# Performance work log

Measured on AMD Instinct MI355X. Metric: run time of the kernel, lower is better.

## Reference

```python
import jax, jax.numpy as jnp
import numpy as np

DIM = 64
NUM_FEAT = 14
NUM_OUT = 105
N_NODES = 8192
N_EDGES = 16384
N_GRAPHS = 256
N_STEMS = 2048
N_JBONDS = 1024


def lrelu(v):
    return jax.nn.leaky_relu(v, 0.01)


def setup_inputs() -> dict:
    key = jax.random.key(0)
    ks = jax.random.split(key, 40)
    def rn(k, shape, s=0.1):
        return jax.random.normal(k, shape, dtype=jnp.float32) * s
    inp = {}
    inp['x'] = jax.random.normal(ks[0], (N_NODES, NUM_FEAT), dtype=jnp.float32)
    inp['edge_attr'] = jax.random.uniform(ks[1], (N_EDGES, 4), dtype=jnp.float32)
    inp['edge_index'] = jax.random.randint(ks[2], (2, N_EDGES), 0, N_NODES)
    inp['batch'] = jnp.sort(jax.random.randint(ks[3], (N_NODES,), 0, N_GRAPHS))
    inp['stem_atmidx'] = jax.random.randint(ks[4], (N_STEMS,), 0, N_NODES)
    inp['jbond_atmidx'] = jax.random.randint(ks[5], (N_JBONDS, 2), 0, N_NODES)
    # lin0
    inp['lin0_w'] = rn(ks[6], (NUM_FEAT, DIM)); inp['lin0_b'] = rn(ks[7], (DIM,))
    # NNConv edge net: Linear(4,dim) -> LeakyReLU -> Linear(dim, dim*dim)
    inp['net_w1'] = rn(ks[8], (4, DIM)); inp['net_b1'] = rn(ks[9], (DIM,))
    inp['net_w2'] = rn(ks[10], (DIM, DIM * DIM), 0.02); inp['net_b2'] = rn(ks[11], (DIM * DIM,), 0.02)
    # NNConv root weight + bias
    inp['conv_root'] = rn(ks[12], (DIM, DIM)); inp['conv_bias'] = rn(ks[13], (DIM,))
    # GRU (torch gate order r,z,n); stored [in, 3*dim]
    inp['gru_w_ih'] = rn(ks[14], (DIM, 3 * DIM)); inp['gru_w_hh'] = rn(ks[15], (DIM, 3 * DIM))
    inp['gru_b_ih'] = rn(ks[16], (3 * DIM,)); inp['gru_b_hh'] = rn(ks[17], (3 * DIM,))
    # node2stem MLP
    inp['n2s_w1'] = rn(ks[18], (DIM, DIM)); inp['n2s_b1'] = rn(ks[19], (DIM,))
    inp['n2s_w2'] = rn(ks[20], (DIM, NUM_OUT)); inp['n2s_b2'] = rn(ks[21], (NUM_OUT,))
    # node2jbond MLP
    inp['n2j_w1'] = rn(ks[22], (DIM, DIM)); inp['n2j_b1'] = rn(ks[23], (DIM,))
    inp['n2j_w2'] = rn(ks[24], (DIM, 1)); inp['n2j_b2'] = rn(ks[25], (1,))
    # Set2Set LSTM(2*dim -> dim), torch gate order i,f,g,o; stored [in, 4*dim]
    inp['s2s_w_ih'] = rn(ks[26], (2 * DIM, 4 * DIM)); inp['s2s_w_hh'] = rn(ks[27], (DIM, 4 * DIM))
    inp['s2s_b_ih'] = rn(ks[28], (4 * DIM,)); inp['s2s_b_hh'] = rn(ks[29], (4 * DIM,))
    # lin_out
    inp['lin_out_w'] = rn(ks[30], (2 * DIM, 2)); inp['lin_out_b'] = rn(ks[31], (2,))
    return inp


def reference(x, edge_attr, lin0_w, lin0_b, net_w1, net_b1, net_w2, net_b2,
              conv_root, conv_bias, gru_w_ih, gru_w_hh, gru_b_ih, gru_b_hh,
              n2s_w1, n2s_b1, n2s_w2, n2s_b2, n2j_w1, n2j_b1, n2j_w2, n2j_b2,
              s2s_w_ih, s2s_w_hh, s2s_b_ih, s2s_b_hh, lin_out_w, lin_out_b,
              edge_index, batch, stem_atmidx, jbond_atmidx):
    N = x.shape[0]
    src, dst = edge_index[0], edge_index[1]
    out = lrelu(x @ lin0_w + lin0_b)          # [N, dim]
    h = out
    # edge-conditioned weights (edge_attr is constant across the 6 iterations)
    ew = (lrelu(edge_attr @ net_w1 + net_b1) @ net_w2 + net_b2).reshape(-1, DIM, DIM)  # [E,dim,dim]
    deg = jnp.maximum(jax.ops.segment_sum(jnp.ones_like(dst, dtype=x.dtype), dst, num_segments=N), 1.0)[:, None]
    for _ in range(6):
        msg = jnp.einsum('ei,eio->eo', out[src], ew)                        # per-edge matmul
        agg = jax.ops.segment_sum(msg, dst, num_segments=N) / deg          # scatter-mean
        m = lrelu(agg + out @ conv_root + conv_bias)
        # GRU update (torch gate order r,z,n)
        gi = m @ gru_w_ih + gru_b_ih
        gh = h @ gru_w_hh + gru_b_hh
        ir, iz, inn = jnp.split(gi, 3, axis=-1)
        hr, hz, hn = jnp.split(gh, 3, axis=-1)
        r = jax.nn.sigmoid(ir + hr)
        z = jax.nn.sigmoid(iz + hz)
        n = jnp.tanh(inn + r * hn)
        h = (1.0 - z) * n + z * h
        out = h
    # per-stem block logits
    stem_preds = lrelu(out[stem_atmidx] @ n2s_w1 + n2s_b1) @ n2s_w2 + n2s_b2  # [S, num_out]
    # jbond: gather both endpoints, predict scalar, mean over the pair
    jb = out[jbond_atmidx.reshape(-1)]
    jpred = lrelu(jb @ n2j_w1 + n2j_b1) @ n2j_w2 + n2j_b2                     # [2J,1]
    jbond_preds = jpred.reshape(jbond_atmidx.shape).mean(axis=1)              # [J]
    # Set2Set, processing_steps=1
    B = N_GRAPHS
    hS = jnp.zeros((B, DIM), x.dtype)
    cS = jnp.zeros((B, DIM), x.dtype)
    q_star = jnp.zeros((B, 2 * DIM), x.dtype)
    gates = q_star @ s2s_w_ih + s2s_b_ih + hS @ s2s_w_hh + s2s_b_hh
    gi_, gf_, gg_, go_ = jnp.split(gates, 4, axis=-1)
    cS = jax.nn.sigmoid(gf_) * cS + jax.nn.sigmoid(gi_) * jnp.tanh(gg_)
    hS = jax.nn.sigmoid(go_) * jnp.tanh(cS)
    q = hS                                                                    # [B, dim]
    e = jnp.sum(out * q[batch], axis=-1)                                      # [N]
    emax = jax.ops.segment_max(e, batch, num_segments=B)
    a_un = jnp.exp(e - emax[batch])
    a = a_un / jax.ops.segment_sum(a_un, batch, num_segments=B)[batch]
    r_pool = jax.ops.segment_sum(a[:, None] * out, batch, num_segments=B)     # [B, dim]
    q_star = jnp.concatenate([q, r_pool], axis=1)                             # [B, 2*dim]
    scalar_outs = q_star @ lin_out_w + lin_out_b                              # [B, 2]
    return (scalar_outs, stem_preds, jbond_preds)
```

## Files before the change

### kernel.cpp

```cpp
#include <hip/hip_runtime.h>

#define DIM 64
#define NF 14
#define NOUT 105
#define NN 8192
#define NE 16384
#define NB 256
#define NS 2048
#define NJ 1024
#define KTOT 4160
#define KSPLIT 8

#define C_X      0
#define C_EA     114688
#define C_L0W    180224
#define C_L0B    181120
#define C_NW1    181184
#define C_NB1    181440
#define C_NW2    181504
#define C_NB2    443648
#define C_CRT    447744
#define C_CB     451840
#define C_GWIH   451904
#define C_GWHH   464192
#define C_GBIH   476480
#define C_GBHH   476672
#define C_SW1    476864
#define C_SB1    480960
#define C_SW2    481024
#define C_SB2    487744
#define C_JW1    487856
#define C_JB1    491952
#define C_JW2    492016
#define C_JB2    492080
#define C_S2IH   492088
#define C_S2HH   492344
#define C_LOW    492600
#define C_LOB    492856
#define C_TOT    492864

typedef float f32x4 __attribute__((ext_vector_type(4)));
typedef short bf16x8 __attribute__((ext_vector_type(8)));

__device__ __forceinline__ float bf2f(unsigned short u){
  union { unsigned int i; float f; } v; v.i = ((unsigned int)u) << 16; return v.f;
}
__device__ __forceinline__ unsigned short f2bf(float f){
  union { float f; unsigned int i; } v; v.f = f;
  unsigned int x = v.i;
  return (unsigned short)((x + 0x7FFFu + ((x >> 16) & 1u)) >> 16);
}
__device__ __forceinline__ float sigm(float x){ return 1.f / (1.f + __expf(-x)); }
__device__ __forceinline__ float tanh_f(float x){
  x = fminf(10.f, fmaxf(-10.f, x));
  float e = __expf(2.f * x);
  return (e - 1.f) / (e + 1.f);
}
__device__ __forceinline__ float lrelu(float x){ return x > 0.f ? x : 0.01f * x; }

__device__ __forceinline__ float wred_sum(float v){
  #pragma unroll
  for (int off = 32; off > 0; off >>= 1) v += __shfl_xor(v, off, 64);
  return v;
}
__device__ __forceinline__ float wred_max(float v){
  #pragma unroll
  for (int off = 32; off > 0; off >>= 1) v = fmaxf(v, __shfl_xor(v, off, 64));
  return v;
}


__global__ void k_detect(const unsigned short* __restrict__ ea, int* __restrict__ flag){
  __shared__ int cnt;
  if (threadIdx.x == 0) cnt = 0;
  __syncthreads();
  int c = 0;
  for (int i = threadIdx.x; i < 8192; i += 256) c += (ea[2*i] >> 15) & 1;
  atomicAdd(&cnt, c);
  __syncthreads();
  if (threadIdx.x == 0) *flag = (cnt > 100) ? 1 : 0;
}

struct CvtArgs {
  const void* src[26];
  int n[26];
  int off[26];
};

__global__ void k_cvt(CvtArgs a, const int* __restrict__ flag, unsigned short* __restrict__ dst){
  bool f32 = (*flag != 0);
  int gid = blockIdx.x * blockDim.x + threadIdx.x, gs = gridDim.x * blockDim.x;
  #pragma unroll 1
  for (int j = 0; j < 26; ++j){
    const void* s = a.src[j];
    int n = a.n[j], o = a.off[j];
    for (int i = gid; i < n; i += gs)
      dst[o + i] = f32 ? f2bf(((const float*)s)[i]) : ((const unsigned short*)s)[i];
  }
}


__global__ void k_deg(const int* __restrict__ ei, float* __restrict__ deg){
  int e = blockIdx.x * blockDim.x + threadIdx.x;
  if (e < NE) atomicAdd(&deg[ei[NE + e]], 1.0f);
}

__global__ void k_lin0(const unsigned short* __restrict__ cvt,
                       float* __restrict__ actF, unsigned short* __restrict__ actB){
  const unsigned short* x = cvt + C_X;
  const unsigned short* w = cvt + C_L0W;
  const unsigned short* b = cvt + C_L0B;
  int idx = blockIdx.x * blockDim.x + threadIdx.x;
  int n = idx >> 6, d = idx & 63;
  float acc = bf2f(b[d]);
  #pragma unroll
  for (int f = 0; f < NF; ++f) acc += bf2f(x[n*NF + f]) * bf2f(w[f*DIM + d]);
  float v = lrelu(acc);
  actF[idx] = v; actB[idx] = f2bf(v);
}

__global__ void k_u(const unsigned short* __restrict__ cvt, unsigned short* __restrict__ u){
  const unsigned short* ea = cvt + C_EA;
  const unsigned short* w  = cvt + C_NW1;
  const unsigned short* b  = cvt + C_NB1;
  int idx = blockIdx.x * blockDim.x + threadIdx.x;
  int e = idx >> 6, d = idx & 63;
  float acc = bf2f(b[d]);
  #pragma unroll
  for (int f = 0; f < 4; ++f) acc += bf2f(ea[e*4 + f]) * bf2f(w[f*DIM + d]);
  u[idx] = f2bf(lrelu(acc));
}

__global__ void k_w2t(const unsigned short* __restrict__ cvt, unsigned short* __restrict__ w2t){
  const unsigned short* w2 = cvt + C_NW2;
  int t = blockIdx.x * blockDim.x + threadIdx.x;
  int n = t >> 6, k = t & 63;
  w2t[t] = w2[k*4096 + n];
}

__global__ void k_w2r(const unsigned short* __restrict__ cvt, unsigned short* __restrict__ w2rt){
  const unsigned short* w2 = cvt + C_NW2;
  const unsigned short* b2 = cvt + C_NB2;
  int t = blockIdx.x * blockDim.x + threadIdx.x;
  int o = t / KTOT, k = t - o * KTOT;
  unsigned short v = (k < 4096) ? w2[(k >> 6) * 4096 + (k & 63) * 64 + o]
                                : b2[(k - 4096) * 64 + o];
  w2rt[t] = v;
}

__global__ void k_prep(const unsigned short* __restrict__ cvt,
                       unsigned short* __restrict__ crt, unsigned short* __restrict__ btg,
                       float* __restrict__ cbg, float* __restrict__ qv){
  const unsigned short* cr  = cvt + C_CRT;
  const unsigned short* wih = cvt + C_GWIH;
  const unsigned short* whh = cvt + C_GWHH;
  const unsigned short* bih = cvt + C_GBIH;
  const unsigned short* bhh = cvt + C_GBHH;
  const unsigned short* s2sbih = cvt + C_S2IH;
  const unsigned short* s2sbhh = cvt + C_S2HH;
  int tid = threadIdx.x;
  for (int t = tid; t < 4096; t += 256){ int n = t & 63, k = t >> 6; crt[n*64 + k] = cr[k*64 + n]; }
  for (int t = tid; t < 32768; t += 256){
    int nidx = t >> 7, kidx = t & 127;
    int g = nidx >> 6, d = nidx & 63, ki = kidx & 63;
    unsigned short v = 0;
    if (kidx < 64){
      if (g == 0) v = wih[ki*192 + d];
      else if (g == 1) v = wih[ki*192 + 64 + d];
      else if (g == 2) v = wih[ki*192 + 128 + d];
    } else {
      if (g == 0) v = whh[ki*192 + d];
      else if (g == 1) v = whh[ki*192 + 64 + d];
      else if (g == 3) v = whh[ki*192 + 128 + d];
    }
    btg[nidx*128 + kidx] = v;
  }
  if (tid < 256){
    int g = tid >> 6, d = tid & 63;
    float v;
    if (g == 0) v = bf2f(bih[d]) + bf2f(bhh[d]);
    else if (g == 1) v = bf2f(bih[64 + d]) + bf2f(bhh[64 + d]);
    else if (g == 2) v = bf2f(bih[128 + d]);
    else v = bf2f(bhh[128 + d]);
    cbg[tid] = v;
  }
  if (tid < 64){
    float gi = bf2f(s2sbih[tid])       + bf2f(s2sbhh[tid]);
    float gg = bf2f(s2sbih[128 + tid]) + bf2f(s2sbhh[128 + tid]);
    float go = bf2f(s2sbih[192 + tid]) + bf2f(s2sbhh[192 + tid]);
    float c = sigm(gi) * tanh_f(gg);
    qv[tid] = sigm(go) * tanh_f(c);
  }
}


__global__ __launch_bounds__(256) void k_ew(const unsigned short* __restrict__ z,
                                            const unsigned short* __restrict__ w2t,
                                            const unsigned short* __restrict__ cvt,
                                            unsigned short* __restrict__ ew){
  const unsigned short* b2 = cvt + C_NB2;
  int w = threadIdx.x >> 6, lane = threadIdx.x & 63;
  int lm = lane & 15, q8 = (lane >> 4) * 8, rq = (lane >> 4) * 4;
  int e0 = blockIdx.x * 64;
  int n0 = blockIdx.y * 256 + w * 64;
  f32x4 acc[4][4];
  #pragma unroll
  for (int mt = 0; mt < 4; ++mt)
    #pragma unroll
    for (int nt = 0; nt < 4; ++nt) acc[mt][nt] = (f32x4){0.f, 0.f, 0.f, 0.f};
  #pragma unroll
  for (int kk = 0; kk < 2; ++kk){
    bf16x8 af[4], bfr[4];
    #pragma unroll
    for (int mt = 0; mt < 4; ++mt)
      af[mt] = *(const bf16x8*)&z[(size_t)(e0 + mt*16 + lm)*64 + kk*32 + q8];
    #pragma unroll
    for (int nt = 0; nt < 4; ++nt)
      bfr[nt] = *(const bf16x8*)&w2t[(size_t)(n0 + nt*16 + lm)*64 + kk*32 + q8];
    #pragma unroll
    for (int mt = 0; mt < 4; ++mt)
      #pragma unroll
      for (int nt = 0; nt < 4; ++nt)
        acc[mt][nt] = __builtin_amdgcn_mfma_f32_16x16x32_bf16(af[mt], bfr[nt], acc[mt][nt], 0, 0, 0);
  }
  #pragma unroll
  for (int nt = 0; nt < 4; ++nt){
    int col = n0 + nt*16 + lm;
    float bb = bf2f(b2[col]);
    #pragma unroll
    for (int mt = 0; mt < 4; ++mt)
      #pragma unroll
      for (int r = 0; r < 4; ++r){
        int row = e0 + mt*16 + rq + r;
        ew[(size_t)row*4096 + col] = f2bf(acc[mt][nt][r] + bb);
      }
  }
}

__global__ __launch_bounds__(256) void k_msg(const unsigned short* __restrict__ actB,
                                             const unsigned short* __restrict__ ew,
                                             const int* __restrict__ ei,
                                             float* __restrict__ agg){
  __shared__ float sact[4][64];
  int w = threadIdx.x >> 6, lane = threadIdx.x & 63;
  int e = blockIdx.x * 4 + w;
  int src = ei[e], dst = ei[NE + e];
  sact[w][lane] = bf2f(actB[(size_t)src*64 + lane]);
  __syncthreads();
  const unsigned short* ep = &ew[(size_t)e * 4096];
  float acc = 0.f;
  #pragma unroll 16
  for (int i = 0; i < 64; ++i) acc += sact[w][i] * bf2f(ep[i*64 + lane]);
  atomicAdd(&agg[(size_t)dst*64 + lane], acc);
}


__global__ __launch_bounds__(256) void k_msgf(const unsigned short* __restrict__ actB,
                                              const unsigned short* __restrict__ z,
                                              const unsigned short* __restrict__ w2rt,
                                              const int* __restrict__ ei,
                                              float* __restrict__ agg){
  __shared__ __align__(16) unsigned short sz[256 * 8];
  int w = threadIdx.x >> 6, lane = threadIdx.x & 63;
  int lm = lane & 15, q8 = (lane >> 4) * 8, rq = (lane >> 4) * 4;
  int e0 = blockIdx.x * 256;
  int s  = blockIdx.y;
  {
    int t = threadIdx.x;
    *(uint4*)&sz[t * 8] = *(const uint4*)&z[(size_t)(e0 + t) * 64 + s * 8];
  }
  __syncthreads();

  uint4 apack[4][2];
  #pragma unroll
  for (int mt = 0; mt < 4; ++mt){
    int src = ei[e0 + w*64 + mt*16 + lm];
    apack[mt][0] = *(const uint4*)&actB[(size_t)src * 64 + q8];
    apack[mt][1] = *(const uint4*)&actB[(size_t)src * 64 + 32 + q8];
  }

  f32x4 acc[4][4];
  #pragma unroll
  for (int mt = 0; mt < 4; ++mt)
    #pragma unroll
    for (int nt = 0; nt < 4; ++nt) acc[mt][nt] = (f32x4){0.f, 0.f, 0.f, 0.f};

  int kk0 = s * 16;
  int nk = (s == KSPLIT - 1) ? 18 : 16;
  for (int c = 0; c < nk; ++c){
    int kk = kk0 + c;
    bf16x8 bfr[4];
    #pragma unroll
    for (int nt = 0; nt < 4; ++nt)
      bfr[nt] = *(const bf16x8*)&w2rt[(size_t)(nt*16 + lm) * KTOT + kk*32 + q8];
    #pragma unroll
    for (int mt = 0; mt < 4; ++mt){
      float zf = 1.0f;
      if (kk < 128){
        int erow = w*64 + mt*16 + lm;
        zf = bf2f(sz[erow * 8 + ((kk >> 1) & 7)]);
      }
      uint4 ap = apack[mt][kk & 1];
      bf16x8 af;
      #pragma unroll
      for (int h = 0; h < 4; ++h){
        unsigned int dw = ((const unsigned int*)&ap)[h];
        float flo = __uint_as_float(dw << 16) * zf;
        float fhi = __uint_as_float(dw & 0xFFFF0000u) * zf;
        unsigned int pk = ((unsigned int)f2bf(flo)) | (((unsigned int)f2bf(fhi)) << 16);
        ((unsigned int*)&af)[h] = pk;
      }
      #pragma unroll
      for (int nt = 0; nt < 4; ++nt)
        acc[mt][nt] = __builtin_amdgcn_mfma_f32_16x16x32_bf16(af, bfr[nt], acc[mt][nt], 0, 0, 0);
    }
  }

  #pragma unroll
  for (int mt = 0; mt < 4; ++mt){
    int dstv[4];
    #pragma unroll
    for (int r = 0; r < 4; ++r) dstv[r] = ei[NE + e0 + w*64 + mt*16 + rq + r];
    #pragma unroll
    for (int nt = 0; nt < 4; ++nt)
      #pragma unroll
      for (int r = 0; r < 4; ++r)
        atomicAdd(&agg[(size_t)dstv[r] * 64 + nt*16 + lm], acc[mt][nt][r]);
  }
}


__global__ __launch_bounds__(256) void k_gru(const unsigned short* __restrict__ actB_in,
                                             const float* __restrict__ actF_in,
                                             float* __restrict__ agg, const float* __restrict__ deg,
                                             const unsigned short* __restrict__ crt,
                                             const unsigned short* __restrict__ cvt,
                                             const unsigned short* __restrict__ btg,
                                             const float* __restrict__ cbg,
                                             float* __restrict__ actF_out, unsigned short* __restrict__ actB_out){
  const unsigned short* cbias = cvt + C_CB;
  __shared__ __align__(16) unsigned short s_frag[2*4*16*8];
  int w = threadIdx.x >> 6, lane = threadIdx.x & 63;
  int lm = lane & 15, q = lane >> 4;
  int q8 = q*8, rq = q*4;
  int r0 = blockIdx.x * 16;
  f32x4 am = (f32x4){0.f, 0.f, 0.f, 0.f};
  #pragma unroll
  for (int kk = 0; kk < 2; ++kk){
    bf16x8 a = *(const bf16x8*)&actB_in[(size_t)(r0 + lm)*64 + kk*32 + q8];
    bf16x8 b = *(const bf16x8*)&crt[(size_t)(w*16 + lm)*64 + kk*32 + q8];
    am = __builtin_amdgcn_mfma_f32_16x16x32_bf16(a, b, am, 0, 0, 0);
  }
  {
    int col = w*16 + lm;
    float cb = bf2f(cbias[col]);
    int kk2 = w >> 1, q2 = (w & 1)*2 + (lm >> 3), j = lm & 7;
    #pragma unroll
    for (int r = 0; r < 4; ++r){
      int row = r0 + rq + r;
      float dg = fmaxf(deg[row], 1.f);
      float v = am[r] + agg[(size_t)row*64 + col] / dg + cb;
      agg[(size_t)row*64 + col] = 0.f;
      s_frag[((kk2*4 + q2)*16 + (rq + r))*8 + j] = f2bf(lrelu(v));
    }
  }
  __syncthreads();
  f32x4 g[4];
  #pragma unroll
  for (int t = 0; t < 4; ++t) g[t] = (f32x4){0.f, 0.f, 0.f, 0.f};
  #pragma unroll
  for (int kk = 0; kk < 4; ++kk){
    bf16x8 a;
    if (kk < 2) a = *(const bf16x8*)&s_frag[(kk*4 + q)*128 + lm*8];
    else        a = *(const bf16x8*)&actB_in[(size_t)(r0 + lm)*64 + (kk - 2)*32 + q8];
    #pragma unroll
    for (int t = 0; t < 4; ++t){
      bf16x8 b = *(const bf16x8*)&btg[(size_t)(t*64 + w*16 + lm)*128 + kk*32 + q8];
      g[t] = __builtin_amdgcn_mfma_f32_16x16x32_bf16(a, b, g[t], 0, 0, 0);
    }
  }
  {
    int d = w*16 + lm;
    float cb_r = cbg[d], cb_z = cbg[64 + d], cb_n = cbg[128 + d], cb_h = cbg[192 + d];
    #pragma unroll
    for (int r = 0; r < 4; ++r){
      int row = r0 + rq + r;
      float rr = sigm(g[0][r] + cb_r);
      float zz = sigm(g[1][r] + cb_z);
      float nn = tanh_f(g[2][r] + cb_n + rr * (g[3][r] + cb_h));
      float ho = actF_in[(size_t)row*64 + d];
      float hn2 = (1.f - zz) * nn + zz * ho;
      actF_out[(size_t)row*64 + d] = hn2;
      actB_out[(size_t)row*64 + d] = f2bf(hn2);
    }
  }
}


__device__ __forceinline__ int lower_bound_batch(const int* b, int val){
  int lo = 0, hi = NN;
  while (lo < hi){ int mid = (lo + hi) >> 1; if (b[mid] < val) lo = mid + 1; else hi = mid; }
  return lo;
}

__device__ __forceinline__ void store_out(void* outp, const int* flag, size_t idx, float v){
  if (*flag) ((float*)outp)[idx] = v;
  else       ((unsigned short*)outp)[idx] = f2bf(v);
}

__global__ __launch_bounds__(64) void k_graph(const float* __restrict__ act,
                                              const int* __restrict__ batch, const float* __restrict__ qv,
                                              const unsigned short* __restrict__ cvt,
                                              const int* __restrict__ flag,
                                              void* __restrict__ outp){
  const unsigned short* lw = cvt + C_LOW;
  const unsigned short* lb = cvt + C_LOB;
  __shared__ float se[512];
  int b = blockIdx.x, lane = threadIdx.x;
  int lo = lower_bound_batch(batch, b);
  int hi = lower_bound_batch(batch, b + 1);
  int cnt = hi - lo; if (cnt > 512) cnt = 512;
  float qvl = qv[lane];
  for (int ii = 0; ii < cnt; ++ii){
    float p = act[(size_t)(lo + ii)*64 + lane] * qvl;
    p = wred_sum(p);
    if (lane == 0) se[ii] = p;
  }
  __syncthreads();
  float em = -3.4e38f;
  for (int ii = lane; ii < cnt; ii += 64) em = fmaxf(em, se[ii]);
  em = wred_max(em);
  float sm = 0.f;
  for (int ii = lane; ii < cnt; ii += 64) sm += __expf(se[ii] - em);
  float denom = wred_sum(sm);
  float rp = 0.f;
  for (int ii = 0; ii < cnt; ++ii) rp += __expf(se[ii] - em) * act[(size_t)(lo + ii)*64 + lane];
  if (cnt > 0 && denom > 0.f) rp /= denom;
  float s0 = qvl*bf2f(lw[lane*2])     + rp*bf2f(lw[(64 + lane)*2]);
  float s1 = qvl*bf2f(lw[lane*2 + 1]) + rp*bf2f(lw[(64 + lane)*2 + 1]);
  s0 = wred_sum(s0); s1 = wred_sum(s1);
  if (lane == 0){
    store_out(outp, flag, b*2,     s0 + bf2f(lb[0]));
    store_out(outp, flag, b*2 + 1, s1 + bf2f(lb[1]));
  }
}

__global__ __launch_bounds__(256) void k_stem(const float* __restrict__ act, const int* __restrict__ sidx,
                                              const unsigned short* __restrict__ cvt,
                                              const int* __restrict__ flag,
                                              void* __restrict__ outp){
  const unsigned short* w1 = cvt + C_SW1;
  const unsigned short* b1 = cvt + C_SB1;
  const unsigned short* w2 = cvt + C_SW2;
  const unsigned short* b2 = cvt + C_SB2;
  __shared__ float sa[4][64], st[4][64];
  int w = threadIdx.x >> 6, lane = threadIdx.x & 63;
  int s = blockIdx.x * 4 + w;
  int a = sidx[s];
  sa[w][lane] = act[(size_t)a*64 + lane];
  __syncthreads();
  float t = bf2f(b1[lane]);
  #pragma unroll 8
  for (int i = 0; i < 64; ++i) t += sa[w][i] * bf2f(w1[i*64 + lane]);
  st[w][lane] = lrelu(t);
  __syncthreads();
  size_t base = 512 + (size_t)s * NOUT;
  float v = bf2f(b2[lane]);
  #pragma unroll 8
  for (int d = 0; d < 64; ++d) v += st[w][d] * bf2f(w2[d*NOUT + lane]);
  store_out(outp, flag, base + lane, v);
  int o2 = 64 + lane;
  if (o2 < NOUT){
    float v2 = bf2f(b2[o2]);
    #pragma unroll 8
    for (int d = 0; d < 64; ++d) v2 += st[w][d] * bf2f(w2[d*NOUT + o2]);
    store_out(outp, flag, base + o2, v2);
  }
}

__global__ __launch_bounds__(256) void k_jbond(const float* __restrict__ act, const int* __restrict__ jidx,
                                               const unsigned short* __restrict__ cvt,
                                               const int* __restrict__ flag,
                                               void* __restrict__ outp){
  const unsigned short* w1 = cvt + C_JW1;
  const unsigned short* b1 = cvt + C_JB1;
  const unsigned short* w2 = cvt + C_JW2;
  const unsigned short* b2 = cvt + C_JB2;
  __shared__ float a0[4][64], a1[4][64];
  int w = threadIdx.x >> 6, lane = threadIdx.x & 63;
  int j = blockIdx.x * 4 + w;
  int i0 = jidx[j*2], i1 = jidx[j*2 + 1];
  a0[w][lane] = act[(size_t)i0*64 + lane];
  a1[w][lane] = act[(size_t)i1*64 + lane];
  __syncthreads();
  float t0 = bf2f(b1[lane]), t1 = t0;
  #pragma unroll 8
  for (int i = 0; i < 64; ++i){
    float wv = bf2f(w1[i*64 + lane]);
    t0 += a0[w][i] * wv;
    t1 += a1[w][i] * wv;
  }
  t0 = lrelu(t0); t1 = lrelu(t1);
  float p = (t0 + t1) * bf2f(w2[lane]);
  p = wred_sum(p);
  if (lane == 0) store_out(outp, flag, 512 + (size_t)NS*NOUT + j, 0.5f * p + bf2f(b2[0]));
}


extern "C" void kernel_launch(void* const* d_in, const int* in_sizes, int n_in,
                              void* d_out, int out_size, void* d_ws, size_t ws_size,
                              hipStream_t stream){
  (void)in_sizes; (void)n_in; (void)out_size;
  const int* edge_index = (const int*)d_in[2];
  const int* batch      = (const int*)d_in[3];
  const int* stem_idx   = (const int*)d_in[4];
  const int* jbond_idx  = (const int*)d_in[5];

  char* ws = (char*)d_ws;
  size_t off = 0;
  auto alloc = [&](size_t bytes) -> void* {
    void* p = ws + off; off += (bytes + 255) & ~(size_t)255; return p;
  };
  unsigned short* cvt  = (unsigned short*)alloc((size_t)C_TOT * 2);
  unsigned short* w2t  = (unsigned short*)alloc((size_t)4096 * 64 * 2);
  unsigned short* w2rt = (unsigned short*)alloc((size_t)64 * KTOT * 2);
  unsigned short* z_bf = (unsigned short*)alloc((size_t)NE * 64 * 2);
  float* actF0 = (float*)alloc((size_t)NN * 64 * 4);
  float* actF1 = (float*)alloc((size_t)NN * 64 * 4);
  unsigned short* actB0 = (unsigned short*)alloc((size_t)NN * 64 * 2);
  unsigned short* actB1 = (unsigned short*)alloc((size_t)NN * 64 * 2);
  float* deg  = (float*)alloc(NN * 4);
  float* agg  = (float*)alloc((size_t)NN * 64 * 4);
  unsigned short* crt = (unsigned short*)alloc(64 * 64 * 2);
  unsigned short* btg = (unsigned short*)alloc(256 * 128 * 2);
  float* cbg  = (float*)alloc(256 * 4);
  float* qv   = (float*)alloc(64 * 4);
  int* flag   = (int*)alloc(256);
  size_t ew_bytes = (size_t)NE * 4096 * 2;
  bool big = (off + ew_bytes) <= ws_size;
  unsigned short* ew = big ? (unsigned short*)alloc(ew_bytes) : nullptr;

  hipMemsetAsync(deg, 0, ((size_t)NN * 4) + ((size_t)NN * 64 * 4) + 256, stream);

  k_detect<<<1, 256, 0, stream>>>((const unsigned short*)d_in[1], flag);

  CvtArgs ca;
  const int srcIdx[26] = {0,1,6,7,8,9,10,11,12,13,14,15,16,17,18,19,20,21,22,23,24,25,28,29,30,31};
  const int ns[26]  = {114688,65536,896,64,256,64,262144,4096,4096,64,12288,12288,192,192,
                       4096,64,6720,105,4096,64,64,1,256,256,256,2};
  const int ofs[26] = {C_X,C_EA,C_L0W,C_L0B,C_NW1,C_NB1,C_NW2,C_NB2,C_CRT,C_CB,C_GWIH,C_GWHH,
                       C_GBIH,C_GBHH,C_SW1,C_SB1,C_SW2,C_SB2,C_JW1,C_JB1,C_JW2,C_JB2,
                       C_S2IH,C_S2HH,C_LOW,C_LOB};
  for (int j = 0; j < 26; ++j){ ca.src[j] = d_in[srcIdx[j]]; ca.n[j] = ns[j]; ca.off[j] = ofs[j]; }
  k_cvt<<<512, 256, 0, stream>>>(ca, flag, cvt);

  k_deg<<<NE/256, 256, 0, stream>>>(edge_index, deg);
  k_lin0<<<NN*DIM/256, 256, 0, stream>>>(cvt, actF0, actB0);
  k_u<<<NE*DIM/256, 256, 0, stream>>>(cvt, z_bf);
  k_prep<<<1, 256, 0, stream>>>(cvt, crt, btg, cbg, qv);

  if (big){
    k_w2t<<<4096*64/256, 256, 0, stream>>>(cvt, w2t);
    k_ew<<<dim3(NE/64, 16), 256, 0, stream>>>(z_bf, w2t, cvt, ew);
  } else {
    k_w2r<<<64*KTOT/256, 256, 0, stream>>>(cvt, w2rt);
  }

  for (int t = 0; t < 6; ++t){
    const float* aF_in  = (t & 1) ? actF1 : actF0;
    float* aF_out       = (t & 1) ? actF0 : actF1;
    const unsigned short* aB_in = (t & 1) ? actB1 : actB0;
    unsigned short* aB_out      = (t & 1) ? actB0 : actB1;
    if (big)
      k_msg<<<NE/4, 256, 0, stream>>>(aB_in, ew, edge_index, agg);
    else
      k_msgf<<<dim3(NE/256, KSPLIT), 256, 0, stream>>>(aB_in, z_bf, w2rt, edge_index, agg);
    k_gru<<<NN/16, 256, 0, stream>>>(aB_in, aF_in, agg, deg, crt, cvt, btg, cbg,
                                     aF_out, aB_out);
  }
  k_graph<<<NB, 64, 0, stream>>>(actF0, batch, qv, cvt, flag, d_out);
  k_stem<<<NS/4, 256, 0, stream>>>(actF0, stem_idx, cvt, flag, d_out);
  k_jbond<<<NJ/4, 256, 0, stream>>>(actF0, jbond_idx, cvt, flag, d_out);
}
```

Before: 444.1 us.

## Permute edge-weight layout for vectorized message loads and fuse setup/head kernels

Transposes the per-edge weight matrix layout (permuted w2t columns and bias index) so the message kernel can read 8 contiguous bf16 values per lane and reduce with shuffles, using fp32 activations instead of bf16 via shared memory. It also merges the five setup kernels into one block-partitioned launch and the three output-head kernels into one launch. The aim is to cut uncoalesced scalar loads in the hot message loop, which runs six times over a 128MB edge-weight tensor, and to reduce launch count. Atomic adds now happen from 8 lanes with 8 values each rather than 64 lanes with one value. The graph head now packs four graphs per block with larger shared memory.

Result: no change. 444.5 us (+0.1%).

```diff
diff --git a/kernel.cpp b/kernel.cpp
--- a/kernel.cpp
+++ b/kernel.cpp
@@ -99,97 +99,98 @@
   }
 }
 
-
-__global__ void k_deg(const int* __restrict__ ei, float* __restrict__ deg){
-  int e = blockIdx.x * blockDim.x + threadIdx.x;
-  if (e < NE) atomicAdd(&deg[ei[NE + e]], 1.0f);
-}
-
-__global__ void k_lin0(const unsigned short* __restrict__ cvt,
-                       float* __restrict__ actF, unsigned short* __restrict__ actB){
-  const unsigned short* x = cvt + C_X;
-  const unsigned short* w = cvt + C_L0W;
-  const unsigned short* b = cvt + C_L0B;
-  int idx = blockIdx.x * blockDim.x + threadIdx.x;
-  int n = idx >> 6, d = idx & 63;
-  float acc = bf2f(b[d]);
-  #pragma unroll
-  for (int f = 0; f < NF; ++f) acc += bf2f(x[n*NF + f]) * bf2f(w[f*DIM + d]);
-  float v = lrelu(acc);
-  actF[idx] = v; actB[idx] = f2bf(v);
-}
-
-__global__ void k_u(const unsigned short* __restrict__ cvt, unsigned short* __restrict__ u){
-  const unsigned short* ea = cvt + C_EA;
-  const unsigned short* w  = cvt + C_NW1;
-  const unsigned short* b  = cvt + C_NB1;
-  int idx = blockIdx.x * blockDim.x + threadIdx.x;
-  int e = idx >> 6, d = idx & 63;
-  float acc = bf2f(b[d]);
-  #pragma unroll
-  for (int f = 0; f < 4; ++f) acc += bf2f(ea[e*4 + f]) * bf2f(w[f*DIM + d]);
-  u[idx] = f2bf(lrelu(acc));
-}
-
-__global__ void k_w2t(const unsigned short* __restrict__ cvt, unsigned short* __restrict__ w2t){
-  const unsigned short* w2 = cvt + C_NW2;
-  int t = blockIdx.x * blockDim.x + threadIdx.x;
-  int n = t >> 6, k = t & 63;
-  w2t[t] = w2[k*4096 + n];
-}
-
-__global__ void k_w2r(const unsigned short* __restrict__ cvt, unsigned short* __restrict__ w2rt){
-  const unsigned short* w2 = cvt + C_NW2;
-  const unsigned short* b2 = cvt + C_NB2;
-  int t = blockIdx.x * blockDim.x + threadIdx.x;
-  int o = t / KTOT, k = t - o * KTOT;
-  unsigned short v = (k < 4096) ? w2[(k >> 6) * 4096 + (k & 63) * 64 + o]
-                                : b2[(k - 4096) * 64 + o];
-  w2rt[t] = v;
-}
-
-__global__ void k_prep(const unsigned short* __restrict__ cvt,
+#define SETUP_BLOCKS 7249
+
+__global__ __launch_bounds__(256) void k_setup(const unsigned short* __restrict__ cvt,
+                       const int* __restrict__ ei, int big,
+                       float* __restrict__ deg,
+                       float* __restrict__ actF, unsigned short* __restrict__ actB,
+                       unsigned short* __restrict__ z,
+                       unsigned short* __restrict__ w2t, unsigned short* __restrict__ w2rt,
                        unsigned short* __restrict__ crt, unsigned short* __restrict__ btg,
                        float* __restrict__ cbg, float* __restrict__ qv){
-  const unsigned short* cr  = cvt + C_CRT;
-  const unsigned short* wih = cvt + C_GWIH;
-  const unsigned short* whh = cvt + C_GWHH;
-  const unsigned short* bih = cvt + C_GBIH;
-  const unsigned short* bhh = cvt + C_GBHH;
-  const unsigned short* s2sbih = cvt + C_S2IH;
-  const unsigned short* s2sbhh = cvt + C_S2HH;
-  int tid = threadIdx.x;
-  for (int t = tid; t < 4096; t += 256){ int n = t & 63, k = t >> 6; crt[n*64 + k] = cr[k*64 + n]; }
-  for (int t = tid; t < 32768; t += 256){
-    int nidx = t >> 7, kidx = t & 127;
-    int g = nidx >> 6, d = nidx & 63, ki = kidx & 63;
-    unsigned short v = 0;
-    if (kidx < 64){
-      if (g == 0) v = wih[ki*192 + d];
-      else if (g == 1) v = wih[ki*192 + 64 + d];
-      else if (g == 2) v = wih[ki*192 + 128 + d];
+  int bid = blockIdx.x, tid = threadIdx.x;
+  if (bid < 2048){
+    const unsigned short* x = cvt + C_X;
+    const unsigned short* w = cvt + C_L0W;
+    const unsigned short* b = cvt + C_L0B;
+    int idx = bid * 256 + tid;
+    int n = idx >> 6, d = idx & 63;
+    float acc = bf2f(b[d]);
+    #pragma unroll
+    for (int f = 0; f < NF; ++f) acc += bf2f(x[n*NF + f]) * bf2f(w[f*DIM + d]);
+    float v = lrelu(acc);
+    actF[idx] = v; actB[idx] = f2bf(v);
+  } else if (bid < 6144){
+    const unsigned short* ea = cvt + C_EA;
+    const unsigned short* w  = cvt + C_NW1;
+    const unsigned short* b  = cvt + C_NB1;
+    int idx = (bid - 2048) * 256 + tid;
+    int e = idx >> 6, d = idx & 63;
+    float acc = bf2f(b[d]);
+    #pragma unroll
+    for (int f = 0; f < 4; ++f) acc += bf2f(ea[e*4 + f]) * bf2f(w[f*DIM + d]);
+    z[idx] = f2bf(lrelu(acc));
+  } else if (bid < 7184){
+    int idx = (bid - 6144) * 256 + tid;
+    const unsigned short* w2 = cvt + C_NW2;
+    if (big){
+      if (idx < 4096*64){
+        int n = idx >> 6, k = idx & 63;
+        int c = ((n & 63) << 6) | (n >> 6);
+        w2t[idx] = w2[k*4096 + c];
+      }
     } else {
-      if (g == 0) v = whh[ki*192 + d];
-      else if (g == 1) v = whh[ki*192 + 64 + d];
-      else if (g == 3) v = whh[ki*192 + 128 + d];
-    }
-    btg[nidx*128 + kidx] = v;
-  }
-  if (tid < 256){
-    int g = tid >> 6, d = tid & 63;
-    float v;
-    if (g == 0) v = bf2f(bih[d]) + bf2f(bhh[d]);
-    else if (g == 1) v = bf2f(bih[64 + d]) + bf2f(bhh[64 + d]);
-    else if (g == 2) v = bf2f(bih[128 + d]);
-    else v = bf2f(bhh[128 + d]);
-    cbg[tid] = v;
-  }
-  if (tid < 64){
-    float gi = bf2f(s2sbih[tid])       + bf2f(s2sbhh[tid]);
-    float gg = bf2f(s2sbih[128 + tid]) + bf2f(s2sbhh[128 + tid]);
-    float go = bf2f(s2sbih[192 + tid]) + bf2f(s2sbhh[192 + tid]);
-    float c = sigm(gi) * tanh_f(gg);
-    qv[tid] = sigm(go) * tanh_f(c);
+      if (idx < 64*KTOT){
+        const unsigned short* b2 = cvt + C_NB2;
+        int o = idx / KTOT, k = idx - o * KTOT;
+        w2rt[idx] = (k < 4096) ? w2[(k >> 6) * 4096 + (k & 63) * 64 + o]
+                               : b2[(k - 4096) * 64 + o];
+      }
+    }
+  } else if (bid < 7248){
+    int e = (bid - 7184) * 256 + tid;
+    if (e < NE) atomicAdd(&deg[ei[NE + e]], 1.0f);
+  } else {
+    const unsigned short* cr  = cvt + C_CRT;
+    const unsigned short* wih = cvt + C_GWIH;
+    const unsigned short* whh = cvt + C_GWHH;
+    const unsigned short* bih = cvt + C_GBIH;
+    const unsigned short* bhh = cvt + C_GBHH;
+    const unsigned short* s2sbih = cvt + C_S2IH;
+    const unsigned short* s2sbhh = cvt + C_S2HH;
+    for (int t = tid; t < 4096; t += 256){ int n = t & 63, k = t >> 6; crt[n*64 + k] = cr[k*64 + n]; }
+    for (int t = tid; t < 32768; t += 256){
+      int nidx = t >> 7, kidx = t & 127;
+      int g = nidx >> 6, d = nidx & 63, ki = kidx & 63;
+      unsigned short v = 0;
+      if (kidx < 64){
+        if (g == 0) v = wih[ki*192 + d];
+        else if (g == 1) v = wih[ki*192 + 64 + d];
+        else if (g == 2) v = wih[ki*192 + 128 + d];
+      } else {
+        if (g == 0) v = whh[ki*192 + d];
+        else if (g == 1) v = whh[ki*192 + 64 + d];
+        else if (g == 3) v = whh[ki*192 + 128 + d];
+      }
+      btg[nidx*128 + kidx] = v;
+    }
+    if (tid < 256){
+      int g = tid >> 6, d = tid & 63;
+      float v;
+      if (g == 0) v = bf2f(bih[d]) + bf2f(bhh[d]);
+      else if (g == 1) v = bf2f(bih[64 + d]) + bf2f(bhh[64 + d]);
+      else if (g == 2) v = bf2f(bih[128 + d]);
+      else v = bf2f(bhh[128 + d]);
+      cbg[tid] = v;
+    }
+    if (tid < 64){
+      float gi = bf2f(s2sbih[tid])       + bf2f(s2sbhh[tid]);
+      float gg = bf2f(s2sbih[128 + tid]) + bf2f(s2sbhh[128 + tid]);
+      float go = bf2f(s2sbih[192 + tid]) + bf2f(s2sbhh[192 + tid]);
+      float c = sigm(gi) * tanh_f(gg);
+      qv[tid] = sigm(go) * tanh_f(c);
+    }
   }
 }
 
@@ -223,35 +224,63 @@
       for (int nt = 0; nt < 4; ++nt)
         acc[mt][nt] = __builtin_amdgcn_mfma_f32_16x16x32_bf16(af[mt], bfr[nt], acc[mt][nt], 0, 0, 0);
   }
+  float bb[4]; int cols[4];
   #pragma unroll
   for (int nt = 0; nt < 4; ++nt){
-    int col = n0 + nt*16 + lm;
-    float bb = bf2f(b2[col]);
-    #pragma unroll
-    for (int mt = 0; mt < 4; ++mt)
+    int dp = n0 + nt*16 + lm;
+    cols[nt] = dp;
+    bb[nt] = bf2f(b2[((dp & 63) << 6) | (dp >> 6)]);
+  }
+  #pragma unroll
+  for (int mt = 0; mt < 4; ++mt)
+    #pragma unroll
+    for (int r = 0; r < 4; ++r){
+      size_t rowb = (size_t)(e0 + mt*16 + rq + r) * 4096;
       #pragma unroll
-      for (int r = 0; r < 4; ++r){
-        int row = e0 + mt*16 + rq + r;
-        ew[(size_t)row*4096 + col] = f2bf(acc[mt][nt][r] + bb);
-      }
-  }
-}
-
-__global__ __launch_bounds__(256) void k_msg(const unsigned short* __restrict__ actB,
+      for (int nt = 0; nt < 4; ++nt)
+        ew[rowb + cols[nt]] = f2bf(acc[mt][nt][r] + bb[nt]);
+    }
+}
+
+__global__ __launch_bounds__(256) void k_msg(const float* __restrict__ actF,
                                              const unsigned short* __restrict__ ew,
                                              const int* __restrict__ ei,
                                              float* __restrict__ agg){
-  __shared__ float sact[4][64];
   int w = threadIdx.x >> 6, lane = threadIdx.x & 63;
   int e = blockIdx.x * 4 + w;
   int src = ei[e], dst = ei[NE + e];
-  sact[w][lane] = bf2f(actB[(size_t)src*64 + lane]);
-  __syncthreads();
-  const unsigned short* ep = &ew[(size_t)e * 4096];
-  float acc = 0.f;
-  #pragma unroll 16
-  for (int i = 0; i < 64; ++i) acc += sact[w][i] * bf2f(ep[i*64 + lane]);
-  atomicAdd(&agg[(size_t)dst*64 + lane], acc);
+  int g = lane >> 3;
+  int s8 = (lane & 7) * 8;
+  f32x4 a0 = *(const f32x4*)&actF[(size_t)src*64 + s8];
+  f32x4 a1 = *(const f32x4*)&actF[(size_t)src*64 + s8 + 4];
+  const unsigned short* ep = ew + (size_t)e * 4096;
+  float po[8];
+  #pragma unroll
+  for (int j = 0; j < 8; ++j){
+    bf16x8 v = *(const bf16x8*)&ep[(size_t)(j*8 + g)*64 + s8];
+    const unsigned int* dw = (const unsigned int*)&v;
+    float acc = 0.f;
+    #pragma unroll
+    for (int h = 0; h < 4; ++h){
+      float flo = __uint_as_float(dw[h] << 16);
+      float fhi = __uint_as_float(dw[h] & 0xFFFF0000u);
+      float alo = (h < 2) ? a0[2*h]     : a1[2*h - 4];
+      float ahi = (h < 2) ? a0[2*h + 1] : a1[2*h - 3];
+      acc += flo * alo + fhi * ahi;
+    }
+    po[j] = acc;
+  }
+  #pragma unroll
+  for (int j = 0; j < 8; ++j){
+    po[j] += __shfl_xor(po[j], 1, 64);
+    po[j] += __shfl_xor(po[j], 2, 64);
+    po[j] += __shfl_xor(po[j], 4, 64);
+  }
+  if ((lane & 7) == 0){
+    #pragma unroll
+    for (int j = 0; j < 8; ++j)
+      atomicAdd(&agg[(size_t)dst*64 + j*8 + g], po[j]);
+  }
 }
 
 
@@ -408,102 +437,97 @@
   else       ((unsigned short*)outp)[idx] = f2bf(v);
 }
 
-__global__ __launch_bounds__(64) void k_graph(const float* __restrict__ act,
-                                              const int* __restrict__ batch, const float* __restrict__ qv,
-                                              const unsigned short* __restrict__ cvt,
-                                              const int* __restrict__ flag,
-                                              void* __restrict__ outp){
-  const unsigned short* lw = cvt + C_LOW;
-  const unsigned short* lb = cvt + C_LOB;
-  __shared__ float se[512];
-  int b = blockIdx.x, lane = threadIdx.x;
-  int lo = lower_bound_batch(batch, b);
-  int hi = lower_bound_batch(batch, b + 1);
-  int cnt = hi - lo; if (cnt > 512) cnt = 512;
-  float qvl = qv[lane];
-  for (int ii = 0; ii < cnt; ++ii){
-    float p = act[(size_t)(lo + ii)*64 + lane] * qvl;
-    p = wred_sum(p);
-    if (lane == 0) se[ii] = p;
-  }
-  __syncthreads();
-  float em = -3.4e38f;
-  for (int ii = lane; ii < cnt; ii += 64) em = fmaxf(em, se[ii]);
-  em = wred_max(em);
-  float sm = 0.f;
-  for (int ii = lane; ii < cnt; ii += 64) sm += __expf(se[ii] - em);
-  float denom = wred_sum(sm);
-  float rp = 0.f;
-  for (int ii = 0; ii < cnt; ++ii) rp += __expf(se[ii] - em) * act[(size_t)(lo + ii)*64 + lane];
-  if (cnt > 0 && denom > 0.f) rp /= denom;
-  float s0 = qvl*bf2f(lw[lane*2])     + rp*bf2f(lw[(64 + lane)*2]);
-  float s1 = qvl*bf2f(lw[lane*2 + 1]) + rp*bf2f(lw[(64 + lane)*2 + 1]);
-  s0 = wred_sum(s0); s1 = wred_sum(s1);
-  if (lane == 0){
-    store_out(outp, flag, b*2,     s0 + bf2f(lb[0]));
-    store_out(outp, flag, b*2 + 1, s1 + bf2f(lb[1]));
-  }
-}
-
-__global__ __launch_bounds__(256) void k_stem(const float* __restrict__ act, const int* __restrict__ sidx,
-                                              const unsigned short* __restrict__ cvt,
-                                              const int* __restrict__ flag,
-                                              void* __restrict__ outp){
-  const unsigned short* w1 = cvt + C_SW1;
-  const unsigned short* b1 = cvt + C_SB1;
-  const unsigned short* w2 = cvt + C_SW2;
-  const unsigned short* b2 = cvt + C_SB2;
-  __shared__ float sa[4][64], st[4][64];
-  int w = threadIdx.x >> 6, lane = threadIdx.x & 63;
-  int s = blockIdx.x * 4 + w;
-  int a = sidx[s];
-  sa[w][lane] = act[(size_t)a*64 + lane];
-  __syncthreads();
-  float t = bf2f(b1[lane]);
-  #pragma unroll 8
-  for (int i = 0; i < 64; ++i) t += sa[w][i] * bf2f(w1[i*64 + lane]);
-  st[w][lane] = lrelu(t);
-  __syncthreads();
-  size_t base = 512 + (size_t)s * NOUT;
-  float v = bf2f(b2[lane]);
-  #pragma unroll 8
-  for (int d = 0; d < 64; ++d) v += st[w][d] * bf2f(w2[d*NOUT + lane]);
-  store_out(outp, flag, base + lane, v);
-  int o2 = 64 + lane;
-  if (o2 < NOUT){
-    float v2 = bf2f(b2[o2]);
-    #pragma unroll 8
-    for (int d = 0; d < 64; ++d) v2 += st[w][d] * bf2f(w2[d*NOUT + o2]);
-    store_out(outp, flag, base + o2, v2);
-  }
-}
-
-__global__ __launch_bounds__(256) void k_jbond(const float* __restrict__ act, const int* __restrict__ jidx,
+__global__ __launch_bounds__(256) void k_heads(const float* __restrict__ act,
+                                               const int* __restrict__ batch,
+                                               const float* __restrict__ qv,
+                                               const int* __restrict__ sidx,
+                                               const int* __restrict__ jidx,
                                                const unsigned short* __restrict__ cvt,
                                                const int* __restrict__ flag,
                                                void* __restrict__ outp){
-  const unsigned short* w1 = cvt + C_JW1;
-  const unsigned short* b1 = cvt + C_JB1;
-  const unsigned short* w2 = cvt + C_JW2;
-  const unsigned short* b2 = cvt + C_JB2;
-  __shared__ float a0[4][64], a1[4][64];
+  int bid = blockIdx.x;
   int w = threadIdx.x >> 6, lane = threadIdx.x & 63;
-  int j = blockIdx.x * 4 + w;
-  int i0 = jidx[j*2], i1 = jidx[j*2 + 1];
-  a0[w][lane] = act[(size_t)i0*64 + lane];
-  a1[w][lane] = act[(size_t)i1*64 + lane];
-  __syncthreads();
-  float t0 = bf2f(b1[lane]), t1 = t0;
-  #pragma unroll 8
-  for (int i = 0; i < 64; ++i){
-    float wv = bf2f(w1[i*64 + lane]);
-    t0 += a0[w][i] * wv;
-    t1 += a1[w][i] * wv;
-  }
-  t0 = lrelu(t0); t1 = lrelu(t1);
-  float p = (t0 + t1) * bf2f(w2[lane]);
-  p = wred_sum(p);
-  if (lane == 0) store_out(outp, flag, 512 + (size_t)NS*NOUT + j, 0.5f * p + bf2f(b2[0]));
+  if (bid < 512){
+    const unsigned short* w1 = cvt + C_SW1;
+    const unsigned short* b1 = cvt + C_SB1;
+    const unsigned short* w2 = cvt + C_SW2;
+    const unsigned short* b2 = cvt + C_SB2;
+    __shared__ float sa[4][64], st[4][64];
+    int s = bid * 4 + w;
+    int a = sidx[s];
+    sa[w][lane] = act[(size_t)a*64 + lane];
+    __syncthreads();
+    float t = bf2f(b1[lane]);
+    #pragma unroll 8
+    for (int i = 0; i < 64; ++i) t += sa[w][i] * bf2f(w1[i*64 + lane]);
+    st[w][lane] = lrelu(t);
+    __syncthreads();
+    size_t base = 512 + (size_t)s * NOUT;
+    float v = bf2f(b2[lane]);
+    #pragma unroll 8
+    for (int d = 0; d < 64; ++d) v += st[w][d] * bf2f(w2[d*NOUT + lane]);
+    store_out(outp, flag, base + lane, v);
+    int o2 = 64 + lane;
+    if (o2 < NOUT){
+      float v2 = bf2f(b2[o2]);
+      #pragma unroll 8
+      for (int d = 0; d < 64; ++d) v2 += st[w][d] * bf2f(w2[d*NOUT + o2]);
+      store_out(outp, flag, base + o2, v2);
+    }
+  } else if (bid < 768){
+    const unsigned short* w1 = cvt + C_JW1;
+    const unsigned short* b1 = cvt + C_JB1;
+    const unsigned short* w2 = cvt + C_JW2;
+    const unsigned short* b2 = cvt + C_JB2;
+    __shared__ float a0[4][64], a1[4][64];
+    int j = (bid - 512) * 4 + w;
+    int i0 = jidx[j*2], i1 = jidx[j*2 + 1];
+    a0[w][lane] = act[(size_t)i0*64 + lane];
+    a1[w][lane] = act[(size_t)i1*64 + lane];
+    __syncthreads();
+    float t0 = bf2f(b1[lane]), t1 = t0;
+    #pragma unroll 8
+    for (int i = 0; i < 64; ++i){
+      float wv = bf2f(w1[i*64 + lane]);
+      t0 += a0[w][i] * wv;
+      t1 += a1[w][i] * wv;
+    }
+    t0 = lrelu(t0); t1 = lrelu(t1);
+    float p = (t0 + t1) * bf2f(w2[lane]);
+    p = wred_sum(p);
+    if (lane == 0) store_out(outp, flag, 512 + (size_t)NS*NOUT + j, 0.5f * p + bf2f(b2[0]));
+  } else {
+    const unsigned short* lw = cvt + C_LOW;
+    const unsigned short* lb = cvt + C_LOB;
+    __shared__ float se[4][512];
+    int b = (bid - 768) * 4 + w;
+    int lo = lower_bound_batch(batch, b);
+    int hi = lower_bound_batch(batch, b + 1);
+    int cnt = hi - lo; if (cnt > 512) cnt = 512;
+    float qvl = qv[lane];
+    for (int ii = 0; ii < cnt; ++ii){
+      float p = act[(size_t)(lo + ii)*64 + lane] * qvl;
+      p = wred_sum(p);
+      if (lane == 0) se[w][ii] = p;
+    }
+    __syncthreads();
+    float em = -3.4e38f;
+    for (int ii = lane; ii < cnt; ii += 64) em = fmaxf(em, se[w][ii]);
+    em = wred_max(em);
+    float sm = 0.f;
+    for (int ii = lane; ii < cnt; ii += 64) sm += __expf(se[w][ii] - em);
+    float denom = wred_sum(sm);
+    float rp = 0.f;
+    for (int ii = 0; ii < cnt; ++ii) rp += __expf(se[w][ii] - em) * act[(size_t)(lo + ii)*64 + lane];
+    if (cnt > 0 && denom > 0.f) rp /= denom;
+    float s0 = qvl*bf2f(lw[lane*2])     + rp*bf2f(lw[(64 + lane)*2]);
+    float s1 = qvl*bf2f(lw[lane*2 + 1]) + rp*bf2f(lw[(64 + lane)*2 + 1]);
+    s0 = wred_sum(s0); s1 = wred_sum(s1);
+    if (lane == 0){
+      store_out(outp, flag, b*2,     s0 + bf2f(lb[0]));
+      store_out(outp, flag, b*2 + 1, s1 + bf2f(lb[1]));
+    }
+  }
 }
 
 
@@ -554,17 +578,12 @@
   for (int j = 0; j < 26; ++j){ ca.src[j] = d_in[srcIdx[j]]; ca.n[j] = ns[j]; ca.off[j] = ofs[j]; }
   k_cvt<<<512, 256, 0, stream>>>(ca, flag, cvt);
 
-  k_deg<<<NE/256, 256, 0, stream>>>(edge_index, deg);
-  k_lin0<<<NN*DIM/256, 256, 0, stream>>>(cvt, actF0, actB0);
-  k_u<<<NE*DIM/256, 256, 0, stream>>>(cvt, z_bf);
-  k_prep<<<1, 256, 0, stream>>>(cvt, crt, btg, cbg, qv);
-
-  if (big){
-    k_w2t<<<4096*64/256, 256, 0, stream>>>(cvt, w2t);
+  k_setup<<<SETUP_BLOCKS, 256, 0, stream>>>(cvt, edge_index, big ? 1 : 0, deg,
+                                            actF0, actB0, z_bf, w2t, w2rt,
+                                            crt, btg, cbg, qv);
+
+  if (big)
     k_ew<<<dim3(NE/64, 16), 256, 0, stream>>>(z_bf, w2t, cvt, ew);
-  } else {
-    k_w2r<<<64*KTOT/256, 256, 0, stream>>>(cvt, w2rt);
-  }
 
   for (int t = 0; t < 6; ++t){
     const float* aF_in  = (t & 1) ? actF1 : actF0;
@@ -572,13 +591,11 @@
     const unsigned short* aB_in = (t & 1) ? actB1 : actB0;
     unsigned short* aB_out      = (t & 1) ? actB0 : actB1;
     if (big)
-      k_msg<<<NE/4, 256, 0, stream>>>(aB_in, ew, edge_index, agg);
+      k_msg<<<NE/4, 256, 0, stream>>>(aF_in, ew, edge_index, agg);
     else
       k_msgf<<<dim3(NE/256, KSPLIT), 256, 0, stream>>>(aB_in, z_bf, w2rt, edge_index, agg);
     k_gru<<<NN/16, 256, 0, stream>>>(aB_in, aF_in, agg, deg, crt, cvt, btg, cbg,
                                      aF_out, aB_out);
   }
-  k_graph<<<NB, 64, 0, stream>>>(actF0, batch, qv, cvt, flag, d_out);
-  k_stem<<<NS/4, 256, 0, stream>>>(actF0, stem_idx, cvt, flag, d_out);
-  k_jbond<<<NJ/4, 256, 0, stream>>>(actF0, jbond_idx, cvt, flag, d_out);
-}
+  k_heads<<<832, 256, 0, stream>>>(actF0, batch, qv, stem_idx, jbond_idx, cvt, flag, d_out);
+}
```
